# Optimization experiments

Measured on AMD Instinct MI355X. Metric: run time of the kernel, lower is better.

## Reference

```python
import jax, jax.numpy as jnp
import numpy as np

SEGMENT_LENGTHS = [1024, 2048, 4096]
DILATION_RATES = [1, 2, 4]


def setup_inputs() -> dict:
    key = jax.random.key(0)
    k1, k2, k3 = jax.random.split(key, 3)
    n = sum(SEGMENT_LENGTHS)  # 7168
    shape = (1, n, 8, 64)  # (b, n, h, d)
    q = jax.random.normal(k1, shape, dtype=jnp.float32)
    k = jax.random.normal(k2, shape, dtype=jnp.float32)
    v = jax.random.normal(k3, shape, dtype=jnp.float32)
    return {"q": q, "k": k, "v": v}


def _attend(q_seg, k_kv, v_kv):
    # q_seg: [b, q_len, h, d]; k_kv/v_kv: [b, k_len, h, d]
    d = q_seg.shape[-1]
    scale = 1.0 / jnp.sqrt(jnp.asarray(d, q_seg.dtype))
    scores = jnp.einsum("bqhd,bkhd->bhqk", q_seg, k_kv) * scale
    w = jax.nn.softmax(scores, axis=-1)
    return jnp.einsum("bhqk,bkhd->bqhd", w, v_kv)


def reference(q, k, v):
    # Single-device dilated attention (ring_size == 1, is_causal=False).
    n = q.shape[1]
    output = jnp.zeros_like(q)
    seg_start = 0
    for seg_len, dilation in zip(SEGMENT_LENGTHS, DILATION_RATES):
        if seg_start >= n:
            break
        seg_end = min(seg_start + seg_len, n)
        q_seg = q[:, seg_start:seg_end]
        if dilation > 1:
            k_d = k[:, ::dilation]
            v_d = v[:, ::dilation]
        else:
            k_d, v_d = k, v
        out_seg = _attend(q_seg, k_d, v_d)
        output = output.at[:, seg_start:seg_end].set(out_seg)
        seg_start = seg_end
    return output
```

## Files before the change

### kernel.cpp

```cpp
#include <hip/hip_runtime.h>

#define VB0 3670016L
#define VB1 7340032L
#define VB2 9175040L
#define PO_OFF 5046272L
#define PL_OFF (PO_OFF + 512L * 128 * 64)

typedef short bvec8 __attribute__((ext_vector_type(8)));
typedef float fvec16 __attribute__((ext_vector_type(16)));

#if defined(__has_builtin)
#if __has_builtin(__builtin_amdgcn_cvt_pk_bf16_f32)
#define HAVE_CVTPK 1
#endif
#if __has_builtin(__builtin_amdgcn_permlane32_swap)
#define HAVE_PLSWAP 1
#endif
#endif

static __device__ __forceinline__ unsigned pk2(float a, float b) {
#ifdef HAVE_CVTPK
  auto r = __builtin_amdgcn_cvt_pk_bf16_f32(a, b);
  unsigned u; __builtin_memcpy(&u, &r, 4);
  return u;
#else
  unsigned ua = (__float_as_uint(a) + 0x8000u) >> 16;
  unsigned ub = (__float_as_uint(b) + 0x8000u) & 0xffff0000u;
  return ua | ub;
#endif
}
static __device__ __forceinline__ void async16(const short* g, short* l) {
  __builtin_amdgcn_global_load_lds((const __attribute__((address_space(1))) unsigned*)(void*)g,
                                   (__attribute__((address_space(3))) unsigned*)(void*)l, 16, 0, 0);
}

__global__ __launch_bounds__(256) void pack_all(const float* __restrict__ k,
                                                const float* __restrict__ v,
                                                short* __restrict__ W) {
  __shared__ float tl[64][65];
  int b = blockIdx.x, t = threadIdx.x;
  if (b < 896) {
    int h = b / 112, tile = b % 112, i0 = tile * 64;
    int r = t >> 2, c = t & 3;
    const float* src = k + ((long)(i0 + r) * 8 + h) * 64 + c * 16;
    short* dst = W + ((long)h * 7168 + i0 + r) * 64 + c * 16;
    union { unsigned u[8]; bvec8 v[2]; } tw;
#pragma unroll
    for (int q4 = 0; q4 < 4; q4++) {
      float4 x = *(const float4*)(src + q4 * 4);
      tw.u[q4 * 2 + 0] = pk2(x.x, x.y);
      tw.u[q4 * 2 + 1] = pk2(x.z, x.w);
    }
    *(bvec8*)dst = tw.v[0];
    *(bvec8*)(dst + 8) = tw.v[1];
  } else {
    int b2 = b - 896;
    int h, tile, dil, L; long base;
    if (b2 < 896)       { L = 7168; dil = 1; h = b2 / 112; tile = b2 % 112; base = VB0; }
    else if (b2 < 1344) { int bb = b2 - 896;  L = 3584; dil = 2; h = bb / 56; tile = bb % 56; base = VB1; }
    else                { int bb = b2 - 1344; L = 1792; dil = 4; h = bb / 28; tile = bb % 28; base = VB2; }
    int i0 = tile * 64;
    int row = t >> 2, c = t & 3;
    const float* src = v + ((long)(i0 + row) * dil * 8 + h) * 64;
#pragma unroll
    for (int cc = 0; cc < 4; cc++) {
      int d0 = c * 16 + cc * 4;
      float4 x = *(const float4*)(src + d0);
      tl[row][d0 + 0] = x.x; tl[row][d0 + 1] = x.y;
      tl[row][d0 + 2] = x.z; tl[row][d0 + 3] = x.w;
    }
    __syncthreads();
    int d = t >> 2, part = t & 3;
    union { unsigned u[8]; bvec8 v[2]; } tw;
#pragma unroll
    for (int u2 = 0; u2 < 8; u2++)
      tw.u[u2] = pk2(tl[part * 16 + 2 * u2][d], tl[part * 16 + 2 * u2 + 1][d]);
    short* dst = W + base + ((long)h * 64 + d) * L + i0 + part * 16;
    *(bvec8*)dst = tw.v[0];
    *(bvec8*)(dst + 8) = tw.v[1];
  }
}

#ifdef HAVE_PLSWAP
#define PEXCH(fu, da0, da1, db0, db1)                                              \
  do {                                                                             \
    auto rr0 = __builtin_amdgcn_permlane32_swap((int)(da0), (int)(db0), false, false); \
    auto rr1 = __builtin_amdgcn_permlane32_swap((int)(da1), (int)(db1), false, false); \
    __builtin_memcpy(&fu.u4[0], &rr0, 4);                                          \
    __builtin_memcpy(&fu.u4[2], (const char*)&rr0 + 4, 4);                         \
    __builtin_memcpy(&fu.u4[1], &rr1, 4);                                          \
    __builtin_memcpy(&fu.u4[3], (const char*)&rr1 + 4, 4);                         \
  } while (0)
#else
#define PEXCH(fu, da0, da1, db0, db1)                                              \
  do {                                                                             \
    unsigned s0 = hb ? (da0) : (db0), s1 = hb ? (da1) : (db1);                     \
    unsigned x0 = __shfl_xor(s0, 32), x1 = __shfl_xor(s1, 32);                     \
    fu.u4[0] = hb ? x0 : (da0);  fu.u4[1] = hb ? x1 : (da1);                       \
    fu.u4[2] = hb ? (db0) : x0;  fu.u4[3] = hb ? (db1) : x1;                       \
  } while (0)
#endif

#define SOFTMAX_PV(KS2)                                                            \
  do {                                                                             \
    const int mb_ = (KS2) >> 1, r0_ = ((KS2) & 1) * 8;                             \
    float p[8];                                                                    \
    _Pragma("unroll") for (int u = 0; u < 8; u++)                                  \
        p[u] = __builtin_amdgcn_exp2f(Sa[mb_][r0_ + u]);                           \
    lacc += ((p[0] + p[1]) + (p[2] + p[3])) + ((p[4] + p[5]) + (p[6] + p[7]));     \
    unsigned da0 = pk2(p[0], p[1]), da1 = pk2(p[2], p[3]);                         \
    unsigned db0 = pk2(p[4], p[5]), db1 = pk2(p[6], p[7]);                         \
    union { unsigned u4[4]; bvec8 v; } fu;                                         \
    PEXCH(fu, da0, da1, db0, db1);                                                 \
    __builtin_amdgcn_s_setprio(1);                                                 \
    Oa[0] = __builtin_amdgcn_mfma_f32_32x32x16_bf16(vf[(KS2)], fu.v, Oa[0], 0, 0, 0);     \
    Oa[1] = __builtin_amdgcn_mfma_f32_32x32x16_bf16(vf[4 + (KS2)], fu.v, Oa[1], 0, 0, 0); \
    __builtin_amdgcn_s_setprio(0);                                                 \
  } while (0)

__global__ __launch_bounds__(256, 3) void attn_kern(const float* __restrict__ q,
                                                    const short* __restrict__ W,
                                                    float* __restrict__ out,
                                                    float* __restrict__ PO,
                                                    float* __restrict__ PL) {
  int b = blockIdx.x;
  int h, q0, dil, kt0, L; long vbo;
  if (b < 256)      { int sp = b & 3; h = (b >> 2) & 7; int qt = b >> 5;
                      q0 = qt * 128;        dil = 1; L = 7168; vbo = VB0; kt0 = sp * 28; }
  else if (b < 512) { int i = b - 256; int sp = i & 1; h = (i >> 1) & 7; int qt = i >> 4;
                      q0 = 1024 + qt * 128; dil = 2; L = 3584; vbo = VB1; kt0 = sp * 28; }
  else              { int i = b - 512; h = i & 7; int qt = i >> 3;
                      q0 = 3072 + qt * 128; dil = 4; L = 1792; vbo = VB2; kt0 = 0; }
  const short* kb = W + (long)h * 7168 * 64;
  const short* vt = W + vbo + (long)h * 64 * L;
  const int dil64 = dil * 64;

  __shared__ __attribute__((aligned(16))) short sK[3][4096];
  __shared__ __attribute__((aligned(16))) short sV[3][4096];
  short* sKf = &sK[0][0];
  short* sVf = &sV[0][0];

  int t = threadIdx.x, lane = t & 63, w = t >> 6;
  int ln = lane & 31, hb = lane >> 5;

  bvec8 qb[4];
  {
    const float* qp = q + ((long)(q0 + w * 32 + ln) * 8 + h) * 64 + 8 * hb;
    const float qs = 0.125f * 1.44269504088896f;
#pragma unroll
    for (int ks = 0; ks < 4; ks++) {
      union { unsigned u[4]; bvec8 v; } qu;
#pragma unroll
      for (int jj = 0; jj < 4; jj++)
        qu.u[jj] = pk2(qs * qp[ks * 16 + 2 * jj], qs * qp[ks * 16 + 2 * jj + 1]);
      qb[ks] = qu.v;
    }
  }

  int srow = lane >> 3, sch = (lane & 7) ^ srow;
  const long kstep = 64L * dil64;
  const short* gk0; const short* gk1; const short* gv0; const short* gv1;
  {
    int row0 = (w * 2 + 0) * 8 + srow, row1 = (w * 2 + 1) * 8 + srow;
    long kb0 = (long)kt0 * 64;
    gk0 = kb + (kb0 + row0) * dil64 + sch * 8;
    gk1 = kb + (kb0 + row1) * dil64 + sch * 8;
    gv0 = vt + (long)row0 * L + kb0 + sch * 8;
    gv1 = vt + (long)row1 * L + kb0 + sch * 8;
  }
  const int ldoff = w * 2 * 512;
  auto stage = [&](int bo2) {
    async16(gk0, sKf + bo2 + ldoff);
    async16(gv0, sVf + bo2 + ldoff);
    async16(gk1, sKf + bo2 + ldoff + 512);
    async16(gv1, sVf + bo2 + ldoff + 512);
    gk0 += kstep; gk1 += kstep; gv0 += 64; gv1 += 64;
  };

  stage(0);
  stage(4096);
  asm volatile("s_waitcnt vmcnt(4)" ::: "memory");
  __builtin_amdgcn_s_barrier();
  asm volatile("" ::: "memory");

  int koff[8];
#pragma unroll
  for (int ks = 0; ks < 4; ks++)
#pragma unroll
    for (int mb = 0; mb < 2; mb++)
      koff[ks * 2 + mb] = (mb * 32 + ln) * 64 + (((2 * ks + hb) ^ (ln & 7)) * 8);

  bvec8 kf[8];
#pragma unroll
  for (int i = 0; i < 8; i++) kf[i] = *(const bvec8*)(sKf + koff[i]);

  fvec16 Oa[2];
  float lacc = 0.f;
#pragma unroll
  for (int i = 0; i < 16; i++) { Oa[0][i] = 0.f; Oa[1][i] = 0.f; }

  int bc = 0, bn = 4096, bs = 8192;
  for (int it = 0; it < 28; it++) {
    bvec8 vf[8];
#pragma unroll
    for (int ks = 0; ks < 4; ks++)
#pragma unroll
      for (int mb = 0; mb < 2; mb++)
        vf[mb * 4 + ks] = *(const bvec8*)(sVf + bc + koff[ks * 2 + mb]);

    fvec16 Sa[2];
#pragma unroll
    for (int i = 0; i < 16; i++) { Sa[0][i] = 0.f; Sa[1][i] = 0.f; }
    __builtin_amdgcn_s_setprio(1);
#pragma unroll
    for (int ks = 0; ks < 4; ks++) {
      Sa[0] = __builtin_amdgcn_mfma_f32_32x32x16_bf16(kf[ks * 2 + 0], qb[ks], Sa[0], 0, 0, 0);
      Sa[1] = __builtin_amdgcn_mfma_f32_32x32x16_bf16(kf[ks * 2 + 1], qb[ks], Sa[1], 0, 0, 0);
    }
    __builtin_amdgcn_s_setprio(0);

    SOFTMAX_PV(0);
    SOFTMAX_PV(1);

    asm volatile("s_waitcnt vmcnt(0)" ::: "memory");
    __builtin_amdgcn_s_barrier();
    asm volatile("" ::: "memory");

    if (it < 26) stage(bs);
    if (it < 27) {
#pragma unroll
      for (int i = 0; i < 8; i++) kf[i] = *(const bvec8*)(sKf + bn + koff[i]);
    }

    SOFTMAX_PV(2);
    SOFTMAX_PV(3);

    bc = bn; bn = bs; bs = (bs == 8192) ? 0 : bs + 4096;
  }

  float lf = lacc + __shfl_xor(lacc, 32);
  int wl = w * 32 + ln;
  if (b < 512) {
    float* po = PO + ((long)b * 128 + wl) * 64;
#pragma unroll
    for (int mb2 = 0; mb2 < 2; mb2++)
#pragma unroll
      for (int r2 = 0; r2 < 4; r2++) {
        float4 x = { Oa[mb2][r2 * 4 + 0], Oa[mb2][r2 * 4 + 1],
                     Oa[mb2][r2 * 4 + 2], Oa[mb2][r2 * 4 + 3] };
        *(float4*)(po + mb2 * 32 + r2 * 8 + hb * 4) = x;
      }
    if (hb == 0) PL[(long)b * 128 + wl] = lf;
  } else {
    float inv = 1.f / lf;
    float* op = out + ((long)(q0 + wl) * 8 + h) * 64;
#pragma unroll
    for (int mb2 = 0; mb2 < 2; mb2++)
#pragma unroll
      for (int r2 = 0; r2 < 4; r2++) {
        float4 x = { Oa[mb2][r2 * 4 + 0] * inv, Oa[mb2][r2 * 4 + 1] * inv,
                     Oa[mb2][r2 * 4 + 2] * inv, Oa[mb2][r2 * 4 + 3] * inv };
        *(float4*)(op + mb2 * 32 + r2 * 8 + hb * 4) = x;
      }
  }
}

__global__ __launch_bounds__(256) void combine_kern(const float* __restrict__ PO,
                                                    const float* __restrict__ PL,
                                                    float* __restrict__ out) {
  int g = blockIdx.x, t = threadIdx.x;
  int base_b, nsp, q0, h;
  if (g < 64) { int qt = g >> 3; h = g & 7; base_b = qt * 32 + h * 4; nsp = 4; q0 = qt * 128; }
  else { int gi = g - 64; int qt = gi >> 3; h = gi & 7; base_b = 256 + qt * 16 + h * 2; nsp = 2; q0 = 1024 + qt * 128; }
  int r = t >> 1, ch = (t & 1) * 32;
  float lt = 0.f;
  for (int sp = 0; sp < nsp; sp++) lt += PL[(long)(base_b + sp) * 128 + r];
  float inv = 1.f / lt;
  float4 acc[8];
#pragma unroll
  for (int j = 0; j < 8; j++) { acc[j].x = 0.f; acc[j].y = 0.f; acc[j].z = 0.f; acc[j].w = 0.f; }
  for (int sp = 0; sp < nsp; sp++) {
    const float4* pb = (const float4*)(PO + ((long)(base_b + sp) * 128 + r) * 64 + ch);
#pragma unroll
    for (int j = 0; j < 8; j++) {
      float4 x = pb[j];
      acc[j].x += x.x; acc[j].y += x.y; acc[j].z += x.z; acc[j].w += x.w;
    }
  }
  float4* op = (float4*)(out + ((long)(q0 + r) * 8 + h) * 64 + ch);
#pragma unroll
  for (int j = 0; j < 8; j++) {
    float4 x = { acc[j].x * inv, acc[j].y * inv, acc[j].z * inv, acc[j].w * inv };
    op[j] = x;
  }
}

extern "C" void kernel_launch(void* const* d_in, const int* in_sizes, int n_in,
                              void* d_out, int out_size, void* d_ws, size_t ws_size,
                              hipStream_t stream) {
  const float* q = (const float*)d_in[0];
  const float* k = (const float*)d_in[1];
  const float* v = (const float*)d_in[2];
  float* out = (float*)d_out;
  short* W = (short*)d_ws;
  float* PO = (float*)d_ws + PO_OFF;
  float* PL = (float*)d_ws + PL_OFF;

  pack_all<<<2464, 256, 0, stream>>>(k, v, W);
  attn_kern<<<768, 256, 0, stream>>>(q, W, out, PO, PL);
  combine_kern<<<192, 256, 0, stream>>>(PO, PL, out);
}
```

Measured before the change: 156.2 us.

## Split each key tile across two wave groups and reduce partial outputs in LDS

Doubles the block to 512 threads so that 8 waves share each 64-key tile. Each of the 4 query-row waves is paired with a second wave, and the two handle different 32-key halves. Each wave does half the QK and PV MFMAs per iteration and holds fewer K/V fragment registers. The partial O accumulators and row sums are then added through shared memory before the final store. The aim is more waves per CU for latency hiding, paid for with an extra LDS reduction and a block-wide sync at the end.

```diff
diff --git a/kernel.cpp b/kernel.cpp
--- a/kernel.cpp
+++ b/kernel.cpp
@@ -101,24 +101,24 @@
   } while (0)
 #endif
 
-#define SOFTMAX_PV(KS2)                                                            \
+#define SOFTMAX_PV(SP)                                                             \
   do {                                                                             \
-    const int mb_ = (KS2) >> 1, r0_ = ((KS2) & 1) * 8;                             \
+    const int r0_ = (SP) * 8;                                                      \
     float p[8];                                                                    \
     _Pragma("unroll") for (int u = 0; u < 8; u++)                                  \
-        p[u] = __builtin_amdgcn_exp2f(Sa[mb_][r0_ + u]);                           \
+        p[u] = __builtin_amdgcn_exp2f(Sa[r0_ + u]);                                \
     lacc += ((p[0] + p[1]) + (p[2] + p[3])) + ((p[4] + p[5]) + (p[6] + p[7]));     \
     unsigned da0 = pk2(p[0], p[1]), da1 = pk2(p[2], p[3]);                         \
     unsigned db0 = pk2(p[4], p[5]), db1 = pk2(p[6], p[7]);                         \
     union { unsigned u4[4]; bvec8 v; } fu;                                         \
     PEXCH(fu, da0, da1, db0, db1);                                                 \
     __builtin_amdgcn_s_setprio(1);                                                 \
-    Oa[0] = __builtin_amdgcn_mfma_f32_32x32x16_bf16(vf[(KS2)], fu.v, Oa[0], 0, 0, 0);     \
-    Oa[1] = __builtin_amdgcn_mfma_f32_32x32x16_bf16(vf[4 + (KS2)], fu.v, Oa[1], 0, 0, 0); \
+    Oa[0] = __builtin_amdgcn_mfma_f32_32x32x16_bf16(vf[(SP)], fu.v, Oa[0], 0, 0, 0);     \
+    Oa[1] = __builtin_amdgcn_mfma_f32_32x32x16_bf16(vf[2 + (SP)], fu.v, Oa[1], 0, 0, 0); \
     __builtin_amdgcn_s_setprio(0);                                                 \
   } while (0)
 
-__global__ __launch_bounds__(256, 3) void attn_kern(const float* __restrict__ q,
+__global__ __launch_bounds__(512, 6) void attn_kern(const float* __restrict__ q,
                                                     const short* __restrict__ W,
                                                     float* __restrict__ out,
                                                     float* __restrict__ PO,
@@ -137,15 +137,17 @@
 
   __shared__ __attribute__((aligned(16))) short sK[3][4096];
   __shared__ __attribute__((aligned(16))) short sV[3][4096];
+  __shared__ float sLm[4][64];
   short* sKf = &sK[0][0];
   short* sVf = &sV[0][0];
 
   int t = threadIdx.x, lane = t & 63, w = t >> 6;
   int ln = lane & 31, hb = lane >> 5;
+  int qh = w & 3, kbh = w >> 2;
 
   bvec8 qb[4];
   {
-    const float* qp = q + ((long)(q0 + w * 32 + ln) * 8 + h) * 64 + 8 * hb;
+    const float* qp = q + ((long)(q0 + qh * 32 + ln) * 8 + h) * 64 + 8 * hb;
     const float qs = 0.125f * 1.44269504088896f;
 #pragma unroll
     for (int ks = 0; ks < 4; ks++) {
@@ -159,40 +161,39 @@
 
   int srow = lane >> 3, sch = (lane & 7) ^ srow;
   const long kstep = 64L * dil64;
-  const short* gk0; const short* gk1; const short* gv0; const short* gv1;
+  const short* gk; const short* gv;
   {
-    int row0 = (w * 2 + 0) * 8 + srow, row1 = (w * 2 + 1) * 8 + srow;
+    int row = w * 8 + srow;
     long kb0 = (long)kt0 * 64;
-    gk0 = kb + (kb0 + row0) * dil64 + sch * 8;
-    gk1 = kb + (kb0 + row1) * dil64 + sch * 8;
-    gv0 = vt + (long)row0 * L + kb0 + sch * 8;
-    gv1 = vt + (long)row1 * L + kb0 + sch * 8;
-  }
-  const int ldoff = w * 2 * 512;
+    gk = kb + (kb0 + row) * dil64 + sch * 8;
+    gv = vt + (long)row * L + kb0 + sch * 8;
+  }
+  const int ldoff = w * 512;
   auto stage = [&](int bo2) {
-    async16(gk0, sKf + bo2 + ldoff);
-    async16(gv0, sVf + bo2 + ldoff);
-    async16(gk1, sKf + bo2 + ldoff + 512);
-    async16(gv1, sVf + bo2 + ldoff + 512);
-    gk0 += kstep; gk1 += kstep; gv0 += 64; gv1 += 64;
+    async16(gk, sKf + bo2 + ldoff);
+    async16(gv, sVf + bo2 + ldoff);
+    gk += kstep; gv += 64;
   };
 
   stage(0);
   stage(4096);
-  asm volatile("s_waitcnt vmcnt(4)" ::: "memory");
+  asm volatile("s_waitcnt vmcnt(2)" ::: "memory");
   __builtin_amdgcn_s_barrier();
   asm volatile("" ::: "memory");
 
-  int koff[8];
+  int koffK[4], koffV[4];
 #pragma unroll
   for (int ks = 0; ks < 4; ks++)
-#pragma unroll
-    for (int mb = 0; mb < 2; mb++)
-      koff[ks * 2 + mb] = (mb * 32 + ln) * 64 + (((2 * ks + hb) ^ (ln & 7)) * 8);
-
-  bvec8 kf[8];
-#pragma unroll
-  for (int i = 0; i < 8; i++) kf[i] = *(const bvec8*)(sKf + koff[i]);
+    koffK[ks] = (kbh * 32 + ln) * 64 + (((2 * ks + hb) ^ (ln & 7)) * 8);
+#pragma unroll
+  for (int dh = 0; dh < 2; dh++)
+#pragma unroll
+    for (int sp = 0; sp < 2; sp++)
+      koffV[dh * 2 + sp] = (dh * 32 + ln) * 64 + (((2 * (2 * kbh + sp) + hb) ^ (ln & 7)) * 8);
+
+  bvec8 kf[4];
+#pragma unroll
+  for (int i = 0; i < 4; i++) kf[i] = *(const bvec8*)(sKf + koffK[i]);
 
   fvec16 Oa[2];
   float lacc = 0.f;
@@ -201,26 +202,20 @@
 
   int bc = 0, bn = 4096, bs = 8192;
   for (int it = 0; it < 28; it++) {
-    bvec8 vf[8];
+    bvec8 vf[4];
+#pragma unroll
+    for (int i = 0; i < 4; i++) vf[i] = *(const bvec8*)(sVf + bc + koffV[i]);
+
+    fvec16 Sa;
+#pragma unroll
+    for (int i = 0; i < 16; i++) Sa[i] = 0.f;
+    __builtin_amdgcn_s_setprio(1);
 #pragma unroll
     for (int ks = 0; ks < 4; ks++)
-#pragma unroll
-      for (int mb = 0; mb < 2; mb++)
-        vf[mb * 4 + ks] = *(const bvec8*)(sVf + bc + koff[ks * 2 + mb]);
-
-    fvec16 Sa[2];
-#pragma unroll
-    for (int i = 0; i < 16; i++) { Sa[0][i] = 0.f; Sa[1][i] = 0.f; }
-    __builtin_amdgcn_s_setprio(1);
-#pragma unroll
-    for (int ks = 0; ks < 4; ks++) {
-      Sa[0] = __builtin_amdgcn_mfma_f32_32x32x16_bf16(kf[ks * 2 + 0], qb[ks], Sa[0], 0, 0, 0);
-      Sa[1] = __builtin_amdgcn_mfma_f32_32x32x16_bf16(kf[ks * 2 + 1], qb[ks], Sa[1], 0, 0, 0);
-    }
+      Sa = __builtin_amdgcn_mfma_f32_32x32x16_bf16(kf[ks], qb[ks], Sa, 0, 0, 0);
     __builtin_amdgcn_s_setprio(0);
 
     SOFTMAX_PV(0);
-    SOFTMAX_PV(1);
 
     asm volatile("s_waitcnt vmcnt(0)" ::: "memory");
     __builtin_amdgcn_s_barrier();
@@ -229,39 +224,60 @@
     if (it < 26) stage(bs);
     if (it < 27) {
 #pragma unroll
-      for (int i = 0; i < 8; i++) kf[i] = *(const bvec8*)(sKf + bn + koff[i]);
-    }
-
-    SOFTMAX_PV(2);
-    SOFTMAX_PV(3);
+      for (int i = 0; i < 4; i++) kf[i] = *(const bvec8*)(sKf + bn + koffK[i]);
+    }
+
+    SOFTMAX_PV(1);
 
     bc = bn; bn = bs; bs = (bs == 8192) ? 0 : bs + 4096;
   }
 
-  float lf = lacc + __shfl_xor(lacc, 32);
-  int wl = w * 32 + ln;
-  if (b < 512) {
-    float* po = PO + ((long)b * 128 + wl) * 64;
-#pragma unroll
-    for (int mb2 = 0; mb2 < 2; mb2++)
-#pragma unroll
-      for (int r2 = 0; r2 < 4; r2++) {
-        float4 x = { Oa[mb2][r2 * 4 + 0], Oa[mb2][r2 * 4 + 1],
-                     Oa[mb2][r2 * 4 + 2], Oa[mb2][r2 * 4 + 3] };
-        *(float4*)(po + mb2 * 32 + r2 * 8 + hb * 4) = x;
-      }
-    if (hb == 0) PL[(long)b * 128 + wl] = lf;
-  } else {
-    float inv = 1.f / lf;
-    float* op = out + ((long)(q0 + wl) * 8 + h) * 64;
-#pragma unroll
-    for (int mb2 = 0; mb2 < 2; mb2++)
-#pragma unroll
-      for (int r2 = 0; r2 < 4; r2++) {
-        float4 x = { Oa[mb2][r2 * 4 + 0] * inv, Oa[mb2][r2 * 4 + 1] * inv,
-                     Oa[mb2][r2 * 4 + 2] * inv, Oa[mb2][r2 * 4 + 3] * inv };
-        *(float4*)(op + mb2 * 32 + r2 * 8 + hb * 4) = x;
-      }
+  float lt = lacc + __shfl_xor(lacc, 32);
+
+  __syncthreads();
+  if (kbh) {
+    float* dst = (qh < 3) ? ((float*)sKf + qh * 2048) : (float*)sVf;
+#pragma unroll
+    for (int dh = 0; dh < 2; dh++)
+#pragma unroll
+      for (int r = 0; r < 16; r++)
+        dst[(dh * 16 + r) * 64 + lane] = Oa[dh][r];
+    sLm[qh][lane] = lt;
+  }
+  __syncthreads();
+  if (!kbh) {
+    const float* src = (qh < 3) ? ((const float*)sKf + qh * 2048) : (const float*)sVf;
+#pragma unroll
+    for (int dh = 0; dh < 2; dh++)
+#pragma unroll
+      for (int r = 0; r < 16; r++)
+        Oa[dh][r] += src[(dh * 16 + r) * 64 + lane];
+    lt += sLm[qh][lane];
+
+    int wl = qh * 32 + ln;
+    if (b < 512) {
+      float* po = PO + ((long)b * 128 + wl) * 64;
+#pragma unroll
+      for (int dh = 0; dh < 2; dh++)
+#pragma unroll
+        for (int r2 = 0; r2 < 4; r2++) {
+          float4 x = { Oa[dh][r2 * 4 + 0], Oa[dh][r2 * 4 + 1],
+                       Oa[dh][r2 * 4 + 2], Oa[dh][r2 * 4 + 3] };
+          *(float4*)(po + dh * 32 + r2 * 8 + hb * 4) = x;
+        }
+      if (hb == 0) PL[(long)b * 128 + wl] = lt;
+    } else {
+      float inv = 1.f / lt;
+      float* op = out + ((long)(q0 + wl) * 8 + h) * 64;
+#pragma unroll
+      for (int dh = 0; dh < 2; dh++)
+#pragma unroll
+        for (int r2 = 0; r2 < 4; r2++) {
+          float4 x = { Oa[dh][r2 * 4 + 0] * inv, Oa[dh][r2 * 4 + 1] * inv,
+                       Oa[dh][r2 * 4 + 2] * inv, Oa[dh][r2 * 4 + 3] * inv };
+          *(float4*)(op + dh * 32 + r2 * 8 + hb * 4) = x;
+        }
+    }
   }
 }
 
@@ -307,6 +323,6 @@
   float* PL = (float*)d_ws + PL_OFF;
 
   pack_all<<<2464, 256, 0, stream>>>(k, v, W);
-  attn_kern<<<768, 256, 0, stream>>>(q, W, out, PO, PL);
+  attn_kern<<<768, 512, 0, stream>>>(q, W, out, PO, PL);
   combine_kern<<<192, 256, 0, stream>>>(PO, PL, out);
 }
```

Result: slower. 341.1 us (+118.4%).

## Double the split-K factor, use fp16 partials and a double-buffered LDS pipeline

Applied to the files above, without the earlier changes.

Raises the KV split for the dilation-1 and dilation-2 segments from 4 and 2 to 8 and 4 splits of 14 tiles each. The grid grows from 768 to 1280 blocks, and the long unsplit dilation-4 blocks are scheduled first. The LDS pipeline drops from triple to double buffering with a __syncthreads per iteration, K fragments are read inside the MFMA loop instead of being prefetched, and occupancy is raised to 5 blocks per CU. Partial outputs and row sums are stored as fp16, halving combine traffic. This risks precision loss from fp16 partial sums and exposes global-load latency through the simpler pipeline.

```diff
diff --git a/kernel.cpp b/kernel.cpp
--- a/kernel.cpp
+++ b/kernel.cpp
@@ -4,10 +4,11 @@
 #define VB1 7340032L
 #define VB2 9175040L
 #define PO_OFF 5046272L
-#define PL_OFF (PO_OFF + 512L * 128 * 64)
 
 typedef short bvec8 __attribute__((ext_vector_type(8)));
 typedef float fvec16 __attribute__((ext_vector_type(16)));
+typedef _Float16 hvec4 __attribute__((ext_vector_type(4)));
+typedef _Float16 hvec8 __attribute__((ext_vector_type(8)));
 
 #if defined(__has_builtin)
 #if __has_builtin(__builtin_amdgcn_cvt_pk_bf16_f32)
@@ -118,25 +119,29 @@
     __builtin_amdgcn_s_setprio(0);                                                 \
   } while (0)
 
-__global__ __launch_bounds__(256, 3) void attn_kern(const float* __restrict__ q,
+__global__ __launch_bounds__(256, 5) void attn_kern(const float* __restrict__ q,
                                                     const short* __restrict__ W,
                                                     float* __restrict__ out,
-                                                    float* __restrict__ PO,
-                                                    float* __restrict__ PL) {
+                                                    _Float16* __restrict__ POh,
+                                                    _Float16* __restrict__ PLh) {
   int b = blockIdx.x;
-  int h, q0, dil, kt0, L; long vbo;
-  if (b < 256)      { int sp = b & 3; h = (b >> 2) & 7; int qt = b >> 5;
-                      q0 = qt * 128;        dil = 1; L = 7168; vbo = VB0; kt0 = sp * 28; }
-  else if (b < 512) { int i = b - 256; int sp = i & 1; h = (i >> 1) & 7; int qt = i >> 4;
-                      q0 = 1024 + qt * 128; dil = 2; L = 3584; vbo = VB1; kt0 = sp * 28; }
-  else              { int i = b - 512; h = i & 7; int qt = i >> 3;
-                      q0 = 3072 + qt * 128; dil = 4; L = 1792; vbo = VB2; kt0 = 0; }
+  int h, q0, dil, kt0, L, NT, pb; long vbo;
+  if (b < 256) {
+    h = b & 7; int qt = b >> 3;
+    q0 = 3072 + qt * 128; dil = 4; L = 1792; vbo = VB2; kt0 = 0; NT = 28; pb = -1;
+  } else if (b < 768) {
+    int i = b - 256; int sp = i & 7; h = (i >> 3) & 7; int qt = i >> 6;
+    q0 = qt * 128; dil = 1; L = 7168; vbo = VB0; kt0 = sp * 14; NT = 14; pb = i;
+  } else {
+    int i = b - 768; int sp = i & 3; h = (i >> 2) & 7; int qt = i >> 5;
+    q0 = 1024 + qt * 128; dil = 2; L = 3584; vbo = VB1; kt0 = sp * 14; NT = 14; pb = 512 + i;
+  }
   const short* kb = W + (long)h * 7168 * 64;
   const short* vt = W + vbo + (long)h * 64 * L;
   const int dil64 = dil * 64;
 
-  __shared__ __attribute__((aligned(16))) short sK[3][4096];
-  __shared__ __attribute__((aligned(16))) short sV[3][4096];
+  __shared__ __attribute__((aligned(16))) short sK[2][4096];
+  __shared__ __attribute__((aligned(16))) short sV[2][4096];
   short* sKf = &sK[0][0];
   short* sVf = &sV[0][0];
 
@@ -178,10 +183,6 @@
   };
 
   stage(0);
-  stage(4096);
-  asm volatile("s_waitcnt vmcnt(4)" ::: "memory");
-  __builtin_amdgcn_s_barrier();
-  asm volatile("" ::: "memory");
 
   int koff[8];
 #pragma unroll
@@ -190,67 +191,59 @@
     for (int mb = 0; mb < 2; mb++)
       koff[ks * 2 + mb] = (mb * 32 + ln) * 64 + (((2 * ks + hb) ^ (ln & 7)) * 8);
 
-  bvec8 kf[8];
-#pragma unroll
-  for (int i = 0; i < 8; i++) kf[i] = *(const bvec8*)(sKf + koff[i]);
-
   fvec16 Oa[2];
   float lacc = 0.f;
 #pragma unroll
   for (int i = 0; i < 16; i++) { Oa[0][i] = 0.f; Oa[1][i] = 0.f; }
 
-  int bc = 0, bn = 4096, bs = 8192;
-  for (int it = 0; it < 28; it++) {
+  int bo = 0;
+  for (int it = 0; it < NT; it++) {
+    __syncthreads();
+    if (it < NT - 1) stage(bo ^ 4096);
+
+    const short* sb = sKf + bo;
+    const short* vb = sVf + bo;
+    bo ^= 4096;
+
     bvec8 vf[8];
 #pragma unroll
     for (int ks = 0; ks < 4; ks++)
 #pragma unroll
       for (int mb = 0; mb < 2; mb++)
-        vf[mb * 4 + ks] = *(const bvec8*)(sVf + bc + koff[ks * 2 + mb]);
+        vf[mb * 4 + ks] = *(const bvec8*)(vb + koff[ks * 2 + mb]);
 
     fvec16 Sa[2];
 #pragma unroll
     for (int i = 0; i < 16; i++) { Sa[0][i] = 0.f; Sa[1][i] = 0.f; }
     __builtin_amdgcn_s_setprio(1);
 #pragma unroll
-    for (int ks = 0; ks < 4; ks++) {
-      Sa[0] = __builtin_amdgcn_mfma_f32_32x32x16_bf16(kf[ks * 2 + 0], qb[ks], Sa[0], 0, 0, 0);
-      Sa[1] = __builtin_amdgcn_mfma_f32_32x32x16_bf16(kf[ks * 2 + 1], qb[ks], Sa[1], 0, 0, 0);
-    }
+    for (int ks = 0; ks < 4; ks++)
+#pragma unroll
+      for (int mb = 0; mb < 2; mb++) {
+        bvec8 kf = *(const bvec8*)(sb + koff[ks * 2 + mb]);
+        Sa[mb] = __builtin_amdgcn_mfma_f32_32x32x16_bf16(kf, qb[ks], Sa[mb], 0, 0, 0);
+      }
     __builtin_amdgcn_s_setprio(0);
 
     SOFTMAX_PV(0);
     SOFTMAX_PV(1);
-
-    asm volatile("s_waitcnt vmcnt(0)" ::: "memory");
-    __builtin_amdgcn_s_barrier();
-    asm volatile("" ::: "memory");
-
-    if (it < 26) stage(bs);
-    if (it < 27) {
-#pragma unroll
-      for (int i = 0; i < 8; i++) kf[i] = *(const bvec8*)(sKf + bn + koff[i]);
-    }
-
     SOFTMAX_PV(2);
     SOFTMAX_PV(3);
-
-    bc = bn; bn = bs; bs = (bs == 8192) ? 0 : bs + 4096;
   }
 
   float lf = lacc + __shfl_xor(lacc, 32);
   int wl = w * 32 + ln;
-  if (b < 512) {
-    float* po = PO + ((long)b * 128 + wl) * 64;
+  if (pb >= 0) {
+    _Float16* po = POh + ((long)pb * 128 + wl) * 64;
 #pragma unroll
     for (int mb2 = 0; mb2 < 2; mb2++)
 #pragma unroll
       for (int r2 = 0; r2 < 4; r2++) {
-        float4 x = { Oa[mb2][r2 * 4 + 0], Oa[mb2][r2 * 4 + 1],
-                     Oa[mb2][r2 * 4 + 2], Oa[mb2][r2 * 4 + 3] };
-        *(float4*)(po + mb2 * 32 + r2 * 8 + hb * 4) = x;
+        hvec4 x = { (_Float16)Oa[mb2][r2 * 4 + 0], (_Float16)Oa[mb2][r2 * 4 + 1],
+                    (_Float16)Oa[mb2][r2 * 4 + 2], (_Float16)Oa[mb2][r2 * 4 + 3] };
+        *(hvec4*)(po + mb2 * 32 + r2 * 8 + hb * 4) = x;
       }
-    if (hb == 0) PL[(long)b * 128 + wl] = lf;
+    if (hb == 0) PLh[(long)pb * 128 + wl] = (_Float16)lf;
   } else {
     float inv = 1.f / lf;
     float* op = out + ((long)(q0 + wl) * 8 + h) * 64;
@@ -265,32 +258,34 @@
   }
 }
 
-__global__ __launch_bounds__(256) void combine_kern(const float* __restrict__ PO,
-                                                    const float* __restrict__ PL,
+__global__ __launch_bounds__(256) void combine_kern(const _Float16* __restrict__ POh,
+                                                    const _Float16* __restrict__ PLh,
                                                     float* __restrict__ out) {
   int g = blockIdx.x, t = threadIdx.x;
-  int base_b, nsp, q0, h;
-  if (g < 64) { int qt = g >> 3; h = g & 7; base_b = qt * 32 + h * 4; nsp = 4; q0 = qt * 128; }
-  else { int gi = g - 64; int qt = gi >> 3; h = gi & 7; base_b = 256 + qt * 16 + h * 2; nsp = 2; q0 = 1024 + qt * 128; }
+  int base, nsp, q0, h;
+  if (g < 64) { int qt = g >> 3; h = g & 7; base = qt * 64 + h * 8; nsp = 8; q0 = qt * 128; }
+  else { int gi = g - 64; int qt = gi >> 3; h = gi & 7; base = 512 + qt * 32 + h * 4; nsp = 4; q0 = 1024 + qt * 128; }
   int r = t >> 1, ch = (t & 1) * 32;
   float lt = 0.f;
-  for (int sp = 0; sp < nsp; sp++) lt += PL[(long)(base_b + sp) * 128 + r];
+  for (int sp = 0; sp < nsp; sp++) lt += (float)PLh[(long)(base + sp) * 128 + r];
   float inv = 1.f / lt;
-  float4 acc[8];
-#pragma unroll
-  for (int j = 0; j < 8; j++) { acc[j].x = 0.f; acc[j].y = 0.f; acc[j].z = 0.f; acc[j].w = 0.f; }
+  float acc[32];
+#pragma unroll
+  for (int j = 0; j < 32; j++) acc[j] = 0.f;
   for (int sp = 0; sp < nsp; sp++) {
-    const float4* pb = (const float4*)(PO + ((long)(base_b + sp) * 128 + r) * 64 + ch);
-#pragma unroll
-    for (int j = 0; j < 8; j++) {
-      float4 x = pb[j];
-      acc[j].x += x.x; acc[j].y += x.y; acc[j].z += x.z; acc[j].w += x.w;
+    const hvec8* pb8 = (const hvec8*)(POh + ((long)(base + sp) * 128 + r) * 64 + ch);
+#pragma unroll
+    for (int j = 0; j < 4; j++) {
+      hvec8 x = pb8[j];
+#pragma unroll
+      for (int kk = 0; kk < 8; kk++) acc[j * 8 + kk] += (float)x[kk];
     }
   }
   float4* op = (float4*)(out + ((long)(q0 + r) * 8 + h) * 64 + ch);
 #pragma unroll
   for (int j = 0; j < 8; j++) {
-    float4 x = { acc[j].x * inv, acc[j].y * inv, acc[j].z * inv, acc[j].w * inv };
+    float4 x = { acc[j * 4 + 0] * inv, acc[j * 4 + 1] * inv,
+                 acc[j * 4 + 2] * inv, acc[j * 4 + 3] * inv };
     op[j] = x;
   }
 }
@@ -303,10 +298,10 @@
   const float* v = (const float*)d_in[2];
   float* out = (float*)d_out;
   short* W = (short*)d_ws;
-  float* PO = (float*)d_ws + PO_OFF;
-  float* PL = (float*)d_ws + PL_OFF;
+  _Float16* POh = (_Float16*)((float*)d_ws + PO_OFF);
+  _Float16* PLh = POh + 1024L * 128 * 64;
 
   pack_all<<<2464, 256, 0, stream>>>(k, v, W);
-  attn_kern<<<768, 256, 0, stream>>>(q, W, out, PO, PL);
-  combine_kern<<<192, 256, 0, stream>>>(PO, PL, out);
-}
+  attn_kern<<<1280, 256, 0, stream>>>(q, W, out, POh, PLh);
+  combine_kern<<<192, 256, 0, stream>>>(POh, PLh, out);
+}
```

Measured after the change: 354.1 us. 2.27x slower.
